# Performance work log

Hardware: AMD Instinct MI355X
Metric: run time of the kernel (lower is better)

Reference implementation:

```python
import jax, jax.numpy as jnp
import numpy as np
import math

HIDDEN = 1024
ADAPTER = 256

def gelu_new(x):
    # BERT/GPT tanh-approx gelu, matches the torch code exactly
    return 0.5 * x * (1.0 + jnp.tanh(math.sqrt(2.0 / math.pi) * (x + 0.044715 * x ** 3)))

def setup_inputs() -> dict:
    key = jax.random.key(0)
    k1, k2, k3 = jax.random.split(key, 3)
    hidden_states = jax.random.normal(k1, (8, 4096, HIDDEN), dtype=jnp.float32)
    # LayerNorm params: weight=1, bias=0 per init_bert_weights
    ln_weight = jnp.ones((HIDDEN,), jnp.float32)
    ln_bias = jnp.zeros((HIDDEN,), jnp.float32)
    # Linear weights ~ N(0, 0.02), biases zero
    w_down = jax.random.normal(k2, (HIDDEN, ADAPTER), jnp.float32) * 0.02
    b_down = jnp.zeros((ADAPTER,), jnp.float32)
    w_up = jax.random.normal(k3, (ADAPTER, HIDDEN), jnp.float32) * 0.02
    b_up = jnp.zeros((HIDDEN,), jnp.float32)
    return {"hidden_states": hidden_states, "ln_weight": ln_weight, "ln_bias": ln_bias,
            "w_down": w_down, "b_down": b_down, "w_up": w_up, "b_up": b_up}

def layer_norm(x, weight, bias, eps=1e-5):
    mean = jnp.mean(x, axis=-1, keepdims=True)
    var = jnp.mean(jnp.square(x - mean), axis=-1, keepdims=True)
    return (x - mean) * jax.lax.rsqrt(var + eps) * weight + bias

def reference(hidden_states, ln_weight, ln_bias, w_down, b_down, w_up, b_up):
    h = layer_norm(hidden_states, ln_weight, ln_bias)           # [B,S,H]
    h = gelu_new(jnp.einsum('bsh,ha->bsa', h, w_down) + b_down)  # [B,S,A]
    h = jnp.einsum('bsa,ah->bsh', h, w_up) + b_up                # [B,S,H]
    return h + hidden_states
```

## Files before the change

### kernel.cpp

```cpp
#include <hip/hip_runtime.h>
#include <hip/hip_bf16.h>

#define HID 1024
#define ADP 256
#define MB  64

typedef short s16x8 __attribute__((ext_vector_type(8)));
typedef float f32x4 __attribute__((ext_vector_type(4)));

__device__ __forceinline__ unsigned short f2bf(float f) {
    union { float f; unsigned int u; } v; v.f = f;
    unsigned int r = v.u + 0x7fffu + ((v.u >> 16) & 1u);
    return (unsigned short)(r >> 16);
}

__device__ __forceinline__ float gelu_new_f(float x) {
    float t = 0.7978845608028654f * x * (1.0f + 0.044715f * x * x);
    t = fminf(fmaxf(t, -15.f), 15.f);
    float e = __expf(-2.0f * t);
    float th = (1.0f - e) / (1.0f + e);
    return 0.5f * x * (1.0f + th);
}

__global__ void transpose_cvt(const float* __restrict__ in, unsigned short* __restrict__ out,
                              int R, int C) {
    __shared__ float t[32][33];
    int r0 = blockIdx.y * 32, c0 = blockIdx.x * 32;
    int tx = threadIdx.x, ty = threadIdx.y;
    #pragma unroll
    for (int j = 0; j < 32; j += 8)
        t[ty + j][tx] = in[(size_t)(r0 + ty + j) * C + c0 + tx];
    __syncthreads();
    #pragma unroll
    for (int j = 0; j < 32; j += 8)
        out[(size_t)(c0 + ty + j) * R + r0 + tx] = f2bf(t[tx][ty + j]);
}

__global__ __launch_bounds__(256, 2)
void adapter_fused(const float* __restrict__ x,
                   const float* __restrict__ lnw, const float* __restrict__ lnb,
                   const float* __restrict__ bdn, const float* __restrict__ bup,
                   const unsigned short* __restrict__ WdT,
                   const unsigned short* __restrict__ WuT,
                   float* __restrict__ out)
{
    __shared__ unsigned short a_h[64][264];
    __shared__ float ep[4][16][68];
    __shared__ float bdn_s[256];
    __shared__ float bup_s[1024];
    __shared__ float stats[64][2];

    const int tid  = threadIdx.x;
    const int wv   = tid >> 6;
    const int lane = tid & 63;
    const int q    = lane >> 4;
    const int l15  = lane & 15;
    const long row0 = (long)blockIdx.x * MB;

    bdn_s[tid] = bdn[tid];
    ((float4*)bup_s)[tid] = ((const float4*)bup)[tid];

    {
        int r = tid >> 2, sub = tid & 3;
        const float4* xr = (const float4*)(x + (row0 + r) * HID);
        float s = 0.f, ss = 0.f;
        #pragma unroll 8
        for (int i = 0; i < 64; ++i) {
            float4 v = xr[sub + 4 * i];
            s  += v.x + v.y + v.z + v.w;
            ss += v.x * v.x + v.y * v.y + v.z * v.z + v.w * v.w;
        }
        s += __shfl_xor(s, 1); ss += __shfl_xor(ss, 1);
        s += __shfl_xor(s, 2); ss += __shfl_xor(ss, 2);
        float mean = s * (1.f / HID);
        float var  = ss * (1.f / HID) - mean * mean;
        if (sub == 0) { stats[r][0] = mean; stats[r][1] = rsqrtf(var + 1e-5f); }
    }
    __syncthreads();

    f32x4 c1[4][4];
    #pragma unroll
    for (int a = 0; a < 4; ++a)
        #pragma unroll
        for (int b = 0; b < 4; ++b)
            c1[a][b] = (f32x4){0.f, 0.f, 0.f, 0.f};

    for (int kc = 0; kc < 4; ++kc) {
        {
            int r = tid >> 2, sub = tid & 3;
            float mean = stats[r][0], rstd = stats[r][1];
            const float4* xr = (const float4*)(x + (row0 + r) * HID + kc * 256);
            const float4* wr = (const float4*)(lnw + kc * 256);
            const float4* br = (const float4*)(lnb + kc * 256);
            #pragma unroll
            for (int i = 0; i < 16; ++i) {
                int f4 = sub + 4 * i;
                float4 v = xr[f4], w4 = wr[f4], b4 = br[f4];
                ushort4 o;
                o.x = f2bf((v.x - mean) * rstd * w4.x + b4.x);
                o.y = f2bf((v.y - mean) * rstd * w4.y + b4.y);
                o.z = f2bf((v.z - mean) * rstd * w4.z + b4.z);
                o.w = f2bf((v.w - mean) * rstd * w4.w + b4.w);
                *(ushort4*)&a_h[r][f4 * 4] = o;
            }
        }
        __syncthreads();
        const int nb = wv * 64;
        #pragma unroll
        for (int ks = 0; ks < 8; ++ks) {
            int kof = ks * 32 + q * 8;
            s16x8 af[4], bfr[4];
            #pragma unroll
            for (int mt = 0; mt < 4; ++mt)
                af[mt] = *(const s16x8*)&a_h[mt * 16 + l15][kof];
            #pragma unroll
            for (int nt = 0; nt < 4; ++nt)
                bfr[nt] = *(const s16x8*)&WdT[(size_t)(nb + nt * 16 + l15) * HID + kc * 256 + kof];
            #pragma unroll
            for (int mt = 0; mt < 4; ++mt)
                #pragma unroll
                for (int nt = 0; nt < 4; ++nt)
                    c1[mt][nt] = __builtin_amdgcn_mfma_f32_16x16x32_bf16(af[mt], bfr[nt], c1[mt][nt], 0, 0, 0);
        }
        __syncthreads();
    }

    #pragma unroll
    for (int mt = 0; mt < 4; ++mt)
        #pragma unroll
        for (int nt = 0; nt < 4; ++nt) {
            int n = wv * 64 + nt * 16 + l15;
            float bd = bdn_s[n];
            #pragma unroll
            for (int r = 0; r < 4; ++r) {
                int m = mt * 16 + q * 4 + r;
                a_h[m][n] = f2bf(gelu_new_f(c1[mt][nt][r] + bd));
            }
        }
    __syncthreads();

    for (int ncc = 0; ncc < 4; ++ncc) {
        const int cb = wv * 256 + ncc * 64;
        f32x4 c2[4][4];
        #pragma unroll
        for (int a = 0; a < 4; ++a)
            #pragma unroll
            for (int b = 0; b < 4; ++b)
                c2[a][b] = (f32x4){0.f, 0.f, 0.f, 0.f};
        #pragma unroll
        for (int ks = 0; ks < 8; ++ks) {
            int kof = ks * 32 + q * 8;
            s16x8 af[4], bfr[4];
            #pragma unroll
            for (int mt = 0; mt < 4; ++mt)
                af[mt] = *(const s16x8*)&a_h[mt * 16 + l15][kof];
            #pragma unroll
            for (int nt = 0; nt < 4; ++nt)
                bfr[nt] = *(const s16x8*)&WuT[(size_t)(cb + nt * 16 + l15) * ADP + kof];
            #pragma unroll
            for (int mt = 0; mt < 4; ++mt)
                #pragma unroll
                for (int nt = 0; nt < 4; ++nt)
                    c2[mt][nt] = __builtin_amdgcn_mfma_f32_16x16x32_bf16(af[mt], bfr[nt], c2[mt][nt], 0, 0, 0);
        }
        #pragma unroll
        for (int mt = 0; mt < 4; ++mt) {
            #pragma unroll
            for (int nt = 0; nt < 4; ++nt)
                #pragma unroll
                for (int r = 0; r < 4; ++r)
                    ep[wv][q * 4 + r][nt * 16 + l15] = c2[mt][nt][r];
            __builtin_amdgcn_s_waitcnt(0xc07f);
            int rr = lane >> 2, c4 = lane & 3;
            long gm = row0 + mt * 16 + rr;
            const float4* xr  = (const float4*)(x + gm * HID + cb);
            float4* orow      = (float4*)(out + gm * HID + cb);
            #pragma unroll
            for (int i = 0; i < 4; ++i) {
                int f4 = i * 4 + c4;
                float4 v  = *(const float4*)&ep[wv][rr][f4 * 4];
                float4 rs = xr[f4];
                float4 bu = *(const float4*)&bup_s[cb + f4 * 4];
                v.x += rs.x + bu.x; v.y += rs.y + bu.y;
                v.z += rs.z + bu.z; v.w += rs.w + bu.w;
                orow[f4] = v;
            }
            __builtin_amdgcn_s_waitcnt(0xc07f);
        }
    }
}

extern "C" void kernel_launch(void* const* d_in, const int* in_sizes, int n_in,
                              void* d_out, int out_size, void* d_ws, size_t ws_size,
                              hipStream_t stream) {
    const float* x   = (const float*)d_in[0];
    const float* lnw = (const float*)d_in[1];
    const float* lnb = (const float*)d_in[2];
    const float* wd  = (const float*)d_in[3];
    const float* bd  = (const float*)d_in[4];
    const float* wu  = (const float*)d_in[5];
    const float* bu  = (const float*)d_in[6];
    float* out = (float*)d_out;

    unsigned short* WdT = (unsigned short*)d_ws;
    unsigned short* WuT = WdT + (size_t)HID * ADP;

    transpose_cvt<<<dim3(ADP / 32, HID / 32), dim3(32, 8), 0, stream>>>(wd, WdT, HID, ADP);
    transpose_cvt<<<dim3(HID / 32, ADP / 32), dim3(32, 8), 0, stream>>>(wu, WuT, ADP, HID);

    const int rows = in_sizes[0] / HID;
    adapter_fused<<<rows / MB, 256, 0, stream>>>(x, lnw, lnb, bd, bu, WdT, WuT, out);
}
```

Measured before the change: 331.2 us.

## Fold LayerNorm into down-projection epilogue and fuse stats into single x pass

The LayerNorm centering and scaling move out of the A-tile fill and into the down-projection epilogue. The fill now converts x*ln_weight to bf16 and accumulates row sum and sum-of-squares in the same pass. Two small precomputed vectors, U = lnw·Wd and V = lnb·Wd + b_down, are built by a new kernel using atomics, which lets the epilogue apply rstd*(acc - mean*U) + V. This removes the separate statistics pass over x. The row tile is also halved to 32 with launch bounds raised to 4 blocks per CU, which improves occupancy but reloads the weights more often. Feeding uncentered values into the bf16 GEMM can reduce precision when row means are large.

Result: slower. 403.1 us (+21.7%).

```diff
diff --git a/kernel.cpp b/kernel.cpp
--- a/kernel.cpp
+++ b/kernel.cpp
@@ -3,7 +3,7 @@
 
 #define HID 1024
 #define ADP 256
-#define MB  64
+#define MB  32
 
 typedef short s16x8 __attribute__((ext_vector_type(8)));
 typedef float f32x4 __attribute__((ext_vector_type(4)));
@@ -36,19 +36,36 @@
         out[(size_t)(c0 + ty + j) * R + r0 + tx] = f2bf(t[tx][ty + j]);
 }
 
-__global__ __launch_bounds__(256, 2)
+__global__ void prep_uv(const float* __restrict__ wd, const float* __restrict__ lnw,
+                        const float* __restrict__ lnb, float* __restrict__ U,
+                        float* __restrict__ V) {
+    int a = threadIdx.x;
+    int h0 = blockIdx.x * 64;
+    float pu = 0.f, pv = 0.f;
+    #pragma unroll 8
+    for (int i = 0; i < 64; ++i) {
+        float w = wd[(size_t)(h0 + i) * ADP + a];
+        pu += lnw[h0 + i] * w;
+        pv += lnb[h0 + i] * w;
+    }
+    atomicAdd(&U[a], pu);
+    atomicAdd(&V[a], pv);
+}
+
+__global__ __launch_bounds__(256, 4)
 void adapter_fused(const float* __restrict__ x,
-                   const float* __restrict__ lnw, const float* __restrict__ lnb,
+                   const float* __restrict__ lnw,
+                   const float* __restrict__ U, const float* __restrict__ V,
                    const float* __restrict__ bdn, const float* __restrict__ bup,
                    const unsigned short* __restrict__ WdT,
                    const unsigned short* __restrict__ WuT,
                    float* __restrict__ out)
 {
-    __shared__ unsigned short a_h[64][264];
-    __shared__ float ep[4][16][68];
-    __shared__ float bdn_s[256];
-    __shared__ float bup_s[1024];
-    __shared__ float stats[64][2];
+    __shared__ unsigned short a_h[32][264];
+    __shared__ float ep[4][16][66];
+    __shared__ float U_s[256];
+    __shared__ float W2_s[256];
+    __shared__ float stats[32][2];
 
     const int tid  = threadIdx.x;
     const int wv   = tid >> 6;
@@ -57,50 +74,34 @@
     const int l15  = lane & 15;
     const long row0 = (long)blockIdx.x * MB;
 
-    bdn_s[tid] = bdn[tid];
-    ((float4*)bup_s)[tid] = ((const float4*)bup)[tid];
-
-    {
-        int r = tid >> 2, sub = tid & 3;
-        const float4* xr = (const float4*)(x + (row0 + r) * HID);
-        float s = 0.f, ss = 0.f;
-        #pragma unroll 8
-        for (int i = 0; i < 64; ++i) {
-            float4 v = xr[sub + 4 * i];
-            s  += v.x + v.y + v.z + v.w;
-            ss += v.x * v.x + v.y * v.y + v.z * v.z + v.w * v.w;
-        }
-        s += __shfl_xor(s, 1); ss += __shfl_xor(ss, 1);
-        s += __shfl_xor(s, 2); ss += __shfl_xor(ss, 2);
-        float mean = s * (1.f / HID);
-        float var  = ss * (1.f / HID) - mean * mean;
-        if (sub == 0) { stats[r][0] = mean; stats[r][1] = rsqrtf(var + 1e-5f); }
-    }
-    __syncthreads();
-
-    f32x4 c1[4][4];
-    #pragma unroll
-    for (int a = 0; a < 4; ++a)
+    U_s[tid]  = U[tid];
+    W2_s[tid] = V[tid] + bdn[tid];
+
+    const int r   = tid >> 3;
+    const int sub = tid & 7;
+
+    f32x4 c1[2][4];
+    #pragma unroll
+    for (int a = 0; a < 2; ++a)
         #pragma unroll
         for (int b = 0; b < 4; ++b)
             c1[a][b] = (f32x4){0.f, 0.f, 0.f, 0.f};
 
+    float s = 0.f, ss = 0.f;
+
     for (int kc = 0; kc < 4; ++kc) {
         {
-            int r = tid >> 2, sub = tid & 3;
-            float mean = stats[r][0], rstd = stats[r][1];
             const float4* xr = (const float4*)(x + (row0 + r) * HID + kc * 256);
             const float4* wr = (const float4*)(lnw + kc * 256);
-            const float4* br = (const float4*)(lnb + kc * 256);
-            #pragma unroll
-            for (int i = 0; i < 16; ++i) {
-                int f4 = sub + 4 * i;
-                float4 v = xr[f4], w4 = wr[f4], b4 = br[f4];
+            #pragma unroll
+            for (int i = 0; i < 8; ++i) {
+                int f4 = sub + 8 * i;
+                float4 v = xr[f4], w4 = wr[f4];
+                s  += v.x + v.y + v.z + v.w;
+                ss += v.x * v.x + v.y * v.y + v.z * v.z + v.w * v.w;
                 ushort4 o;
-                o.x = f2bf((v.x - mean) * rstd * w4.x + b4.x);
-                o.y = f2bf((v.y - mean) * rstd * w4.y + b4.y);
-                o.z = f2bf((v.z - mean) * rstd * w4.z + b4.z);
-                o.w = f2bf((v.w - mean) * rstd * w4.w + b4.w);
+                o.x = f2bf(v.x * w4.x); o.y = f2bf(v.y * w4.y);
+                o.z = f2bf(v.z * w4.z); o.w = f2bf(v.w * w4.w);
                 *(ushort4*)&a_h[r][f4 * 4] = o;
             }
         }
@@ -109,15 +110,15 @@
         #pragma unroll
         for (int ks = 0; ks < 8; ++ks) {
             int kof = ks * 32 + q * 8;
-            s16x8 af[4], bfr[4];
-            #pragma unroll
-            for (int mt = 0; mt < 4; ++mt)
+            s16x8 af[2], bfr[4];
+            #pragma unroll
+            for (int mt = 0; mt < 2; ++mt)
                 af[mt] = *(const s16x8*)&a_h[mt * 16 + l15][kof];
             #pragma unroll
             for (int nt = 0; nt < 4; ++nt)
                 bfr[nt] = *(const s16x8*)&WdT[(size_t)(nb + nt * 16 + l15) * HID + kc * 256 + kof];
             #pragma unroll
-            for (int mt = 0; mt < 4; ++mt)
+            for (int mt = 0; mt < 2; ++mt)
                 #pragma unroll
                 for (int nt = 0; nt < 4; ++nt)
                     c1[mt][nt] = __builtin_amdgcn_mfma_f32_16x16x32_bf16(af[mt], bfr[nt], c1[mt][nt], 0, 0, 0);
@@ -125,62 +126,76 @@
         __syncthreads();
     }
 
-    #pragma unroll
-    for (int mt = 0; mt < 4; ++mt)
+    s += __shfl_xor(s, 1); ss += __shfl_xor(ss, 1);
+    s += __shfl_xor(s, 2); ss += __shfl_xor(ss, 2);
+    s += __shfl_xor(s, 4); ss += __shfl_xor(ss, 4);
+    if (sub == 0) {
+        float mean = s * (1.f / HID);
+        float var  = ss * (1.f / HID) - mean * mean;
+        stats[r][0] = mean;
+        stats[r][1] = rsqrtf(var + 1e-5f);
+    }
+    __syncthreads();
+
+    #pragma unroll
+    for (int mt = 0; mt < 2; ++mt)
         #pragma unroll
         for (int nt = 0; nt < 4; ++nt) {
             int n = wv * 64 + nt * 16 + l15;
-            float bd = bdn_s[n];
-            #pragma unroll
-            for (int r = 0; r < 4; ++r) {
-                int m = mt * 16 + q * 4 + r;
-                a_h[m][n] = f2bf(gelu_new_f(c1[mt][nt][r] + bd));
+            float u = U_s[n], w2 = W2_s[n];
+            #pragma unroll
+            for (int rr = 0; rr < 4; ++rr) {
+                int m = mt * 16 + q * 4 + rr;
+                float mean = stats[m][0], rstd = stats[m][1];
+                float val = rstd * c1[mt][nt][rr] - rstd * mean * u + w2;
+                a_h[m][n] = f2bf(gelu_new_f(val));
             }
         }
     __syncthreads();
 
     for (int ncc = 0; ncc < 4; ++ncc) {
         const int cb = wv * 256 + ncc * 64;
-        f32x4 c2[4][4];
-        #pragma unroll
-        for (int a = 0; a < 4; ++a)
+        f32x4 c2[2][4];
+        #pragma unroll
+        for (int a = 0; a < 2; ++a)
             #pragma unroll
             for (int b = 0; b < 4; ++b)
                 c2[a][b] = (f32x4){0.f, 0.f, 0.f, 0.f};
         #pragma unroll
         for (int ks = 0; ks < 8; ++ks) {
             int kof = ks * 32 + q * 8;
-            s16x8 af[4], bfr[4];
-            #pragma unroll
-            for (int mt = 0; mt < 4; ++mt)
+            s16x8 af[2], bfr[4];
+            #pragma unroll
+            for (int mt = 0; mt < 2; ++mt)
                 af[mt] = *(const s16x8*)&a_h[mt * 16 + l15][kof];
             #pragma unroll
             for (int nt = 0; nt < 4; ++nt)
                 bfr[nt] = *(const s16x8*)&WuT[(size_t)(cb + nt * 16 + l15) * ADP + kof];
             #pragma unroll
-            for (int mt = 0; mt < 4; ++mt)
+            for (int mt = 0; mt < 2; ++mt)
                 #pragma unroll
                 for (int nt = 0; nt < 4; ++nt)
                     c2[mt][nt] = __builtin_amdgcn_mfma_f32_16x16x32_bf16(af[mt], bfr[nt], c2[mt][nt], 0, 0, 0);
         }
         #pragma unroll
-        for (int mt = 0; mt < 4; ++mt) {
+        for (int mt = 0; mt < 2; ++mt) {
             #pragma unroll
             for (int nt = 0; nt < 4; ++nt)
                 #pragma unroll
-                for (int r = 0; r < 4; ++r)
-                    ep[wv][q * 4 + r][nt * 16 + l15] = c2[mt][nt][r];
+                for (int rr = 0; rr < 4; ++rr)
+                    ep[wv][q * 4 + rr][nt * 16 + l15] = c2[mt][nt][rr];
             __builtin_amdgcn_s_waitcnt(0xc07f);
-            int rr = lane >> 2, c4 = lane & 3;
-            long gm = row0 + mt * 16 + rr;
-            const float4* xr  = (const float4*)(x + gm * HID + cb);
-            float4* orow      = (float4*)(out + gm * HID + cb);
+            int er = lane >> 2, c4 = lane & 3;
+            long gm = row0 + mt * 16 + er;
+            const float4* xr = (const float4*)(x + gm * HID + cb);
+            const float4* br = (const float4*)(bup + cb);
+            float4* orow     = (float4*)(out + gm * HID + cb);
             #pragma unroll
             for (int i = 0; i < 4; ++i) {
                 int f4 = i * 4 + c4;
-                float4 v  = *(const float4*)&ep[wv][rr][f4 * 4];
+                float4 v  = *(const float4*)&ep[wv][er][f4 * 4];
                 float4 rs = xr[f4];
-                float4 bu = *(const float4*)&bup_s[cb + f4 * 4];
+                float4 bu = br[f4];
                 v.x += rs.x + bu.x; v.y += rs.y + bu.y;
                 v.z += rs.z + bu.z; v.w += rs.w + bu.w;
                 orow[f4] = v;
@@ -204,10 +219,15 @@
 
     unsigned short* WdT = (unsigned short*)d_ws;
     unsigned short* WuT = WdT + (size_t)HID * ADP;
+    float* U = (float*)(WuT + (size_t)HID * ADP);
+    float* V = U + ADP;
+
+    hipMemsetAsync(U, 0, 2 * ADP * sizeof(float), stream);
+    prep_uv<<<HID / 64, ADP, 0, stream>>>(wd, lnw, lnb, U, V);
 
     transpose_cvt<<<dim3(ADP / 32, HID / 32), dim3(32, 8), 0, stream>>>(wd, WdT, HID, ADP);
     transpose_cvt<<<dim3(HID / 32, ADP / 32), dim3(32, 8), 0, stream>>>(wu, WuT, ADP, HID);
 
     const int rows = in_sizes[0] / HID;
-    adapter_fused<<<rows / MB, 256, 0, stream>>>(x, lnw, lnb, bd, bu, WdT, WuT, out);
-}
+    adapter_fused<<<rows / MB, 256, 0, stream>>>(x, lnw, U, V, bd, bu, WdT, WuT, out);
+}
```
